# Kernel tuning notes

Hardware: AMD Instinct MI355X
Metric: run time of the kernel (lower is better)

Reference implementation:

```python
import jax, jax.numpy as jnp
import numpy as np


def setup_inputs() -> dict:
    key = jax.random.key(0)
    ks = jax.random.split(key, 6)
    B, N, F = 32, 2048, 64
    C1, C2, H = 32, 32, 512
    x = jax.random.normal(ks[0], (B, N, F), dtype=jnp.float32)
    a = jax.random.uniform(ks[1], (B, N, N), dtype=jnp.float32)
    W1 = jax.random.normal(ks[2], (F, C1), dtype=jnp.float32) * (1.0 / np.sqrt(F))
    b1 = jnp.zeros((C1,), dtype=jnp.float32)
    W2 = jax.random.normal(ks[3], (C1, C2), dtype=jnp.float32) * (1.0 / np.sqrt(C1))
    b2 = jnp.zeros((C2,), dtype=jnp.float32)
    Wf1 = jax.random.normal(ks[4], (C2, H), dtype=jnp.float32) * (1.0 / np.sqrt(C2))
    bf1 = jnp.zeros((H,), dtype=jnp.float32)
    Wf2 = jax.random.normal(ks[5], (H, 1), dtype=jnp.float32) * (1.0 / np.sqrt(H))
    bf2 = jnp.zeros((1,), dtype=jnp.float32)
    return {"x": x, "a": a, "W1": W1, "b1": b1, "W2": W2, "b2": b2,
            "Wf1": Wf1, "bf1": bf1, "Wf2": Wf2, "bf2": bf2}


def _gcn(x, a, W, b):
    # GCNConv batch mode: act(A @ X @ W + b); project first (cheaper: F -> C)
    xw = jnp.einsum('bnf,fc->bnc', x, W)
    return jax.nn.relu(jnp.einsum('bnm,bmc->bnc', a, xw) + b)


def reference(x, a, W1, b1, W2, b2, Wf1, bf1, Wf2, bf2):
    h = _gcn(x, a, W1, b1)          # [B,N,32]
    h = _gcn(h, a, W2, b2)          # [B,N,32]
    pooled = jnp.sum(h, axis=1)     # GlobalSumPool over nodes -> [B,32]
    h = jax.nn.relu(pooled @ Wf1 + bf1)  # [B,512]
    out = h @ Wf2 + bf2             # linear output activation -> [B,1]
    return out
```

## Files before the change

kernel.cpp:

```cpp
#include <hip/hip_runtime.h>

using bf16x8 = __attribute__((ext_vector_type(8))) short;
using f32x4  = __attribute__((ext_vector_type(4))) float;

static constexpr int NN = 2048;
static constexpr int NB = 32;
static constexpr int NC = 32;

__device__ __forceinline__ unsigned short f2bf(float f) {
    unsigned int u = __float_as_uint(f);
    u += 0x7FFFu + ((u >> 16) & 1u);
    return (unsigned short)(u >> 16);
}

template<int INCH>
__global__ void proj_kernel(const float* __restrict__ X, const float* __restrict__ W,
                            unsigned short* __restrict__ XWt)
{
    __shared__ float wlds[INCH * NC];
    const int b = blockIdx.y;
    const int m = blockIdx.x * 256 + threadIdx.x;
    for (int i = threadIdx.x; i < INCH * NC; i += 256) wlds[i] = W[i];
    __syncthreads();

    const float* xrow = X + ((size_t)b * NN + m) * INCH;
    float acc[NC];
#pragma unroll
    for (int c = 0; c < NC; ++c) acc[c] = 0.f;

    for (int f = 0; f < INCH; f += 4) {
        const float4 v = *reinterpret_cast<const float4*>(xrow + f);
        const float xv[4] = {v.x, v.y, v.z, v.w};
#pragma unroll
        for (int j = 0; j < 4; ++j) {
#pragma unroll
            for (int c = 0; c < NC; ++c)
                acc[c] += xv[j] * wlds[(f + j) * NC + c];
        }
    }

    unsigned short* outp = XWt + (size_t)b * NC * NN + m;
#pragma unroll
    for (int c = 0; c < NC; ++c) outp[(size_t)c * NN] = f2bf(acc[c]);
}

template<bool WRITE_H>
__global__ void gcn_gemm(const float* __restrict__ A, const unsigned short* __restrict__ Bt,
                         const float* __restrict__ bias, float* __restrict__ Hout,
                         float* __restrict__ pooled)
{
    const int b    = blockIdx.y;
    const int wave = threadIdx.x >> 6;
    const int lane = threadIdx.x & 63;
    const int lr   = lane & 15;
    const int kg   = lane >> 4;

    const int r0 = blockIdx.x * 64 + wave * 16;

    const float*          ap  = A  + ((size_t)b * NN + (r0 + lr)) * NN + kg * 8;
    const unsigned short* bp0 = Bt + ((size_t)b * NC + lr) * NN + kg * 8;
    const unsigned short* bp1 = bp0 + (size_t)16 * NN;

    f32x4 acc0 = {0.f, 0.f, 0.f, 0.f};
    f32x4 acc1 = {0.f, 0.f, 0.f, 0.f};

    const int k0 = ((blockIdx.x + 37 * blockIdx.y) & 63) << 5;

    auto kstep = [&](int k) {
        const float4 x0 = *reinterpret_cast<const float4*>(ap + k);
        const float4 x1 = *reinterpret_cast<const float4*>(ap + k + 4);
        const bf16x8 bv0 = *reinterpret_cast<const bf16x8*>(bp0 + k);
        const bf16x8 bv1 = *reinterpret_cast<const bf16x8*>(bp1 + k);

        bf16x8 af;
        af[0] = (short)f2bf(x0.x); af[1] = (short)f2bf(x0.y);
        af[2] = (short)f2bf(x0.z); af[3] = (short)f2bf(x0.w);
        af[4] = (short)f2bf(x1.x); af[5] = (short)f2bf(x1.y);
        af[6] = (short)f2bf(x1.z); af[7] = (short)f2bf(x1.w);

        acc0 = __builtin_amdgcn_mfma_f32_16x16x32_bf16(af, bv0, acc0, 0, 0, 0);
        acc1 = __builtin_amdgcn_mfma_f32_16x16x32_bf16(af, bv1, acc1, 0, 0, 0);
    };

#pragma unroll 2
    for (int k = k0; k < NN; k += 32) kstep(k);
#pragma unroll 2
    for (int k = 0; k < k0; k += 32) kstep(k);

    const float bias0 = bias[lr];
    const float bias1 = bias[lr + 16];

    if constexpr (WRITE_H) {
#pragma unroll
        for (int j = 0; j < 4; ++j) {
            const int row = r0 + kg * 4 + j;
            float* hp = Hout + ((size_t)b * NN + row) * NC;
            hp[lr]      = fmaxf(acc0[j] + bias0, 0.f);
            hp[lr + 16] = fmaxf(acc1[j] + bias1, 0.f);
        }
    } else {
        float s0 = 0.f, s1 = 0.f;
#pragma unroll
        for (int j = 0; j < 4; ++j) {
            s0 += fmaxf(acc0[j] + bias0, 0.f);
            s1 += fmaxf(acc1[j] + bias1, 0.f);
        }
        s0 += __shfl_xor(s0, 16); s0 += __shfl_xor(s0, 32);
        s1 += __shfl_xor(s1, 16); s1 += __shfl_xor(s1, 32);
        if (kg == 0) {
            atomicAdd(&pooled[b * NC + lr],      s0);
            atomicAdd(&pooled[b * NC + 16 + lr], s1);
        }
    }
}

__global__ void head_kernel(const float* __restrict__ pooled,
                            const float* __restrict__ Wf1, const float* __restrict__ bf1,
                            const float* __restrict__ Wf2, const float* __restrict__ bf2,
                            float* __restrict__ out)
{
    const int b = blockIdx.x;
    const int h = threadIdx.x;

    float dot = 0.f;
#pragma unroll
    for (int c = 0; c < NC; ++c)
        dot += pooled[b * NC + c] * Wf1[c * 512 + h];

    const float v   = fmaxf(dot + bf1[h], 0.f);
    float part      = v * Wf2[h];

#pragma unroll
    for (int off = 32; off >= 1; off >>= 1)
        part += __shfl_xor(part, off);

    __shared__ float red[8];
    if ((threadIdx.x & 63) == 0) red[threadIdx.x >> 6] = part;
    __syncthreads();
    if (threadIdx.x == 0) {
        float s = 0.f;
#pragma unroll
        for (int i = 0; i < 8; ++i) s += red[i];
        out[b] = s + bf2[0];
    }
}

extern "C" void kernel_launch(void* const* d_in, const int* in_sizes, int n_in,
                              void* d_out, int out_size, void* d_ws, size_t ws_size,
                              hipStream_t stream)
{
    const float* x   = (const float*)d_in[0];
    const float* a   = (const float*)d_in[1];
    const float* W1  = (const float*)d_in[2];
    const float* b1  = (const float*)d_in[3];
    const float* W2  = (const float*)d_in[4];
    const float* b2  = (const float*)d_in[5];
    const float* Wf1 = (const float*)d_in[6];
    const float* bf1 = (const float*)d_in[7];
    const float* Wf2 = (const float*)d_in[8];
    const float* bf2 = (const float*)d_in[9];
    float* out = (float*)d_out;

    char* ws = (char*)d_ws;
    unsigned short* xwt1 = (unsigned short*)(ws);
    float*          h1   = (float*)(ws + (4ull << 20));
    unsigned short* xwt2 = (unsigned short*)(ws + (12ull << 20));
    float*          pooled = (float*)(ws + (16ull << 20));

    hipMemsetAsync(pooled, 0, NB * NC * sizeof(float), stream);

    dim3 pgrid(NN / 256, NB);
    proj_kernel<64><<<pgrid, 256, 0, stream>>>(x, W1, xwt1);

    dim3 ggrid(NN / 64, NB);
    gcn_gemm<true><<<ggrid, 256, 0, stream>>>(a, xwt1, b1, h1, nullptr);

    proj_kernel<32><<<pgrid, 256, 0, stream>>>(h1, W2, xwt2);

    gcn_gemm<false><<<ggrid, 256, 0, stream>>>(a, xwt2, b2, nullptr, pooled);

    head_kernel<<<dim3(NB), 512, 0, stream>>>(pooled, Wf1, bf1, Wf2, bf2, out);
}
```

Measured before the change: 291.5 us.

## Reverse K order in second GCN pass and use intrinsic bf16 conversion

Removes the per-block staggered K start and replaces it with a plain forward sweep in the first GCN GEMM and a backward sweep in the second. Reading A in reverse order in the second pass is meant to reuse the tail of A still in the large last-level cache from the first pass. The unroll factor goes from 2 to 4, and the hand-written float-to-bf16 rounding is replaced with the HIP __float2bfloat16 intrinsic. In exchange it drops the channel/bank staggering that the rotated start offset provided, so many blocks may contend on the same addresses.

```diff
diff --git a/kernel.cpp b/kernel.cpp
--- a/kernel.cpp
+++ b/kernel.cpp
@@ -1,4 +1,5 @@
 #include <hip/hip_runtime.h>
+#include <hip/hip_bf16.h>
 
 using bf16x8 = __attribute__((ext_vector_type(8))) short;
 using f32x4  = __attribute__((ext_vector_type(4))) float;
@@ -44,7 +45,7 @@
     for (int c = 0; c < NC; ++c) outp[(size_t)c * NN] = f2bf(acc[c]);
 }
 
-template<bool WRITE_H>
+template<bool WRITE_H, bool REVK>
 __global__ void gcn_gemm(const float* __restrict__ A, const unsigned short* __restrict__ Bt,
                          const float* __restrict__ bias, float* __restrict__ Hout,
                          float* __restrict__ pooled)
@@ -64,7 +65,7 @@
     f32x4 acc0 = {0.f, 0.f, 0.f, 0.f};
     f32x4 acc1 = {0.f, 0.f, 0.f, 0.f};
 
-    const int k0 = ((blockIdx.x + 37 * blockIdx.y) & 63) << 5;
+    union ABf { bf16x8 v; __hip_bfloat16 e[8]; };
 
     auto kstep = [&](int k) {
         const float4 x0 = *reinterpret_cast<const float4*>(ap + k);
@@ -72,20 +73,23 @@
         const bf16x8 bv0 = *reinterpret_cast<const bf16x8*>(bp0 + k);
         const bf16x8 bv1 = *reinterpret_cast<const bf16x8*>(bp1 + k);
 
-        bf16x8 af;
-        af[0] = (short)f2bf(x0.x); af[1] = (short)f2bf(x0.y);
-        af[2] = (short)f2bf(x0.z); af[3] = (short)f2bf(x0.w);
-        af[4] = (short)f2bf(x1.x); af[5] = (short)f2bf(x1.y);
-        af[6] = (short)f2bf(x1.z); af[7] = (short)f2bf(x1.w);
+        ABf af;
+        af.e[0] = __float2bfloat16(x0.x); af.e[1] = __float2bfloat16(x0.y);
+        af.e[2] = __float2bfloat16(x0.z); af.e[3] = __float2bfloat16(x0.w);
+        af.e[4] = __float2bfloat16(x1.x); af.e[5] = __float2bfloat16(x1.y);
+        af.e[6] = __float2bfloat16(x1.z); af.e[7] = __float2bfloat16(x1.w);
 
-        acc0 = __builtin_amdgcn_mfma_f32_16x16x32_bf16(af, bv0, acc0, 0, 0, 0);
-        acc1 = __builtin_amdgcn_mfma_f32_16x16x32_bf16(af, bv1, acc1, 0, 0, 0);
+        acc0 = __builtin_amdgcn_mfma_f32_16x16x32_bf16(af.v, bv0, acc0, 0, 0, 0);
+        acc1 = __builtin_amdgcn_mfma_f32_16x16x32_bf16(af.v, bv1, acc1, 0, 0, 0);
     };
 
-#pragma unroll 2
-    for (int k = k0; k < NN; k += 32) kstep(k);
-#pragma unroll 2
-    for (int k = 0; k < k0; k += 32) kstep(k);
+    if constexpr (REVK) {
+#pragma unroll 4
+        for (int k = NN - 32; k >= 0; k -= 32) kstep(k);
+    } else {
+#pragma unroll 4
+        for (int k = 0; k < NN; k += 32) kstep(k);
+    }
 
     const float bias0 = bias[lr];
     const float bias1 = bias[lr + 16];
@@ -169,15 +173,15 @@
 
     hipMemsetAsync(pooled, 0, NB * NC * sizeof(float), stream);
 
-    dim3 pgrid(NN / 256, NB);
-    proj_kernel<64><<<pgrid, 256, 0, stream>>>(x, W1, xwt1);
+    proj_kernel<64><<<dim3(NN / 256, NB), 256, 0, stream>>>(x, W1, xwt1);
 
-    dim3 ggrid(NN / 64, NB);
-    gcn_gemm<true><<<ggrid, 256, 0, stream>>>(a, xwt1, b1, h1, nullptr);
+    gcn_gemm<true, false><<<dim3(NN / 64, NB), 256, 0, stream>>>(
+        a, xwt1, b1, h1, nullptr);
 
-    proj_kernel<32><<<pgrid, 256, 0, stream>>>(h1, W2, xwt2);
+    proj_kernel<32><<<dim3(NN / 256, NB), 256, 0, stream>>>(h1, W2, xwt2);
 
-    gcn_gemm<false><<<ggrid, 256, 0, stream>>>(a, xwt2, b2, nullptr, pooled);
+    gcn_gemm<false, true><<<dim3(NN / 64, NB), 256, 0, stream>>>(
+        a, xwt2, b2, nullptr, pooled);
 
     head_kernel<<<dim3(NB), 512, 0, stream>>>(pooled, Wf1, bf1, Wf2, bf2, out);
 }
```

Measured after the change: 289.6 us. No clear change (-0.6%).
